# Optimization experiments

Measured on AMD Instinct MI355X. Metric: run time of the kernel, lower is better.

Reference implementation:

```python
import jax, jax.numpy as jnp
import numpy as np

EPS = 1e-5

def _layernorm(x, g, b):
    mu = jnp.mean(x, axis=-1, keepdims=True)
    var = jnp.mean((x - mu) ** 2, axis=-1, keepdims=True)
    return (x - mu) * jax.lax.rsqrt(var + EPS) * g + b

def setup_inputs() -> dict:
    key = jax.random.key(0)
    ks = jax.random.split(key, 12)
    B, N, C, n = 2, 1024, 256, 100
    x = jax.random.normal(ks[0], (B, N, C), dtype=jnp.float32)
    query = jax.random.normal(ks[1], (n, B, C), dtype=jnp.float32)
    policy = jax.random.uniform(ks[2], (B, N, 1), dtype=jnp.float32)
    s = lambda k, shp: jax.random.normal(k, shp, dtype=jnp.float32) * (1.0 / np.sqrt(shp[0]))
    return {
        "x": x, "query": query, "policy": policy,
        "ln_g": jnp.ones((C,), jnp.float32), "ln_b": jnp.zeros((C,), jnp.float32),
        "W_in": s(ks[3], (C, C)), "b_in": jnp.zeros((C,), jnp.float32),
        "W1": s(ks[4], (2 * C, C)), "b1": jnp.zeros((C,), jnp.float32),
        "W2": s(ks[5], (C, C // 2)), "b2": jnp.zeros((C // 2,), jnp.float32),
        "W3": s(ks[6], (C // 2, 2)), "b3": jnp.zeros((2,), jnp.float32),
    }

def reference(x, query, policy, ln_g, ln_b, W_in, b_in, W1, b1, W2, b2, W3, b3):
    B, N, C = x.shape
    n = query.shape[0]
    q = jnp.transpose(query, (1, 0, 2))  # [B, n, C]
    # in_conv: LayerNorm -> Linear -> GELU. The torch code repeats x across the
    # query dim first, but the math is identical per query, so compute once.
    h = jax.nn.gelu(_layernorm(x, ln_g, ln_b) @ W_in + b_in, approximate=False)  # [B, N, C]
    half = C // 2
    local_x = h[:, :, :half]  # [B, N, C/2]
    # policy-weighted masked pooling (policy identical across queries)
    glob = jnp.sum(h[:, :, half:] * policy, axis=1, keepdims=True) / jnp.sum(policy, axis=1, keepdims=True)  # [B, 1, C/2]
    feature = jnp.concatenate([
        jnp.broadcast_to(local_x[:, None, :, :], (B, n, N, half)),
        jnp.broadcast_to(glob[:, None, :, :], (B, n, N, half)),
        jnp.broadcast_to(q[:, :, None, :], (B, n, N, C)),
    ], axis=-1)  # [B, n, N, 2C]
    z = jax.nn.gelu(feature @ W1 + b1, approximate=False)
    z = jax.nn.gelu(z @ W2 + b2, approximate=False)
    z = z @ W3 + b3
    return jax.nn.log_softmax(z, axis=-1)  # [B, n, N, 2]
```

## Files before the change

### kernel.cpp

```cpp
#include <hip/hip_runtime.h>
#include <hip/hip_bf16.h>
#include <math.h>

#define BB 2
#define NN 1024
#define CC 256
#define NQ 100
#define HALF 128

typedef __attribute__((ext_vector_type(8))) short bf16x8;
typedef __attribute__((ext_vector_type(4))) float f32x4;

__device__ __forceinline__ float exp2_fast(float v) {
#if __has_builtin(__builtin_amdgcn_exp2f)
    return __builtin_amdgcn_exp2f(v);
#else
    return __expf(0.69314718056f * v);
#endif
}

__device__ __forceinline__ float gelu_fast(float x) {
    float x2 = x * x;
    float v = x * fmaf(0.10293942f, x2, 2.30211418f);
    float e = exp2_fast(v);
    float r = __builtin_amdgcn_rcpf(1.0f + e);
    return fmaf(-x, r, x);
}

__device__ __forceinline__ short f2bf(float f) {
    union { float f; unsigned u; } v; v.f = f;
    return (short)((v.u + 0x7FFFu + ((v.u >> 16) & 1u)) >> 16);
}

__global__ __launch_bounds__(256) void kA_fused(
        const float* __restrict__ x, const float* __restrict__ ln_g,
        const float* __restrict__ ln_b, const float* __restrict__ W_in,
        const float* __restrict__ b_in, const float* __restrict__ policy,
        const float* __restrict__ W1, float* __restrict__ At,
        float* __restrict__ gpart, float* __restrict__ ppart) {
    __shared__ float xst[CC][4];
    __shared__ float hst[HALF][4];
    int t = threadIdx.x;
    int wave = t >> 6, lane = t & 63;
    int blk = blockIdx.x;
    int row0 = blk * 4;
    const float* xr = x + (size_t)(row0 + wave) * CC;
    float v0 = xr[lane], v1 = xr[lane + 64], v2 = xr[lane + 128], v3 = xr[lane + 192];
    float s = v0 + v1 + v2 + v3;
    for (int off = 32; off; off >>= 1) s += __shfl_down(s, off);
    s = __shfl(s, 0);
    float mu = s * (1.0f / CC);
    float d0 = v0 - mu, d1 = v1 - mu, d2 = v2 - mu, d3 = v3 - mu;
    float vs = d0 * d0 + d1 * d1 + d2 * d2 + d3 * d3;
    for (int off = 32; off; off >>= 1) vs += __shfl_down(vs, off);
    vs = __shfl(vs, 0);
    float rstd = rsqrtf(vs * (1.0f / CC) + 1e-5f);
    xst[lane][wave]       = d0 * rstd * ln_g[lane]       + ln_b[lane];
    xst[lane + 64][wave]  = d1 * rstd * ln_g[lane + 64]  + ln_b[lane + 64];
    xst[lane + 128][wave] = d2 * rstd * ln_g[lane + 128] + ln_b[lane + 128];
    xst[lane + 192][wave] = d3 * rstd * ln_g[lane + 192] + ln_b[lane + 192];
    __syncthreads();
    float a0 = b_in[t], a1 = a0, a2 = a0, a3 = a0;
    #pragma unroll 8
    for (int k = 0; k < CC; ++k) {
        float4 xv = *(const float4*)xst[k];
        float wv = W_in[k * CC + t];
        a0 = fmaf(xv.x, wv, a0); a1 = fmaf(xv.y, wv, a1);
        a2 = fmaf(xv.z, wv, a2); a3 = fmaf(xv.w, wv, a3);
    }
    float h0 = gelu_fast(a0), h1 = gelu_fast(a1);
    float h2 = gelu_fast(a2), h3 = gelu_fast(a3);
    float p0 = policy[row0], p1 = policy[row0 + 1];
    float p2 = policy[row0 + 2], p3 = policy[row0 + 3];
    if (t < HALF) {
        hst[t][0] = h0; hst[t][1] = h1; hst[t][2] = h2; hst[t][3] = h3;
    } else {
        gpart[(size_t)blk * HALF + (t - HALF)] =
            h0 * p0 + h1 * p1 + h2 * p2 + h3 * p3;
    }
    if (t == 0) ppart[blk] = p0 + p1 + p2 + p3;
    __syncthreads();
    float c0 = 0, c1 = 0, c2 = 0, c3 = 0;
    #pragma unroll 8
    for (int k = 0; k < HALF; ++k) {
        float4 hv = *(const float4*)hst[k];
        float wv = W1[k * CC + t];
        c0 = fmaf(hv.x, wv, c0); c1 = fmaf(hv.y, wv, c1);
        c2 = fmaf(hv.z, wv, c2); c3 = fmaf(hv.w, wv, c3);
    }
    int b = row0 >> 10;
    int lr = row0 & (NN - 1);
    size_t tb = ((size_t)(b * 64 + (lr >> 4)) * 32 + (t >> 3)) * 128 + (t & 7);
    int r16 = lr & 15;
    At[tb + (r16 + 0) * 8] = c0;
    At[tb + (r16 + 1) * 8] = c1;
    At[tb + (r16 + 2) * 8] = c2;
    At[tb + (r16 + 3) * 8] = c3;
}

__global__ __launch_bounds__(256) void kB_qc_prep(
        const float* __restrict__ query, const float* __restrict__ W1,
        const float* __restrict__ W2, const float* __restrict__ gpart,
        const float* __restrict__ ppart, const float* __restrict__ b1,
        float* __restrict__ Qc, short* __restrict__ W2T) {
    int blk = blockIdx.x, t = threadIdx.x;
    if (blk >= BB * NQ) {
        int u = (blk - BB * NQ) * 256 + t;
        int n = u & 127;
        int kq = u >> 7;
        short4 v;
        v.x = f2bf(W2[(kq * 4 + 0) * HALF + n]);
        v.y = f2bf(W2[(kq * 4 + 1) * HALF + n]);
        v.z = f2bf(W2[(kq * 4 + 2) * HALF + n]);
        v.w = f2bf(W2[(kq * 4 + 3) * HALF + n]);
        *(short4*)(W2T + (size_t)((n >> 4) * 32 + (kq >> 1)) * 128
                   + (n & 15) * 8 + (kq & 1) * 4) = v;
        return;
    }
    __shared__ float gl2[2][HALF];
    __shared__ float gls[HALF];
    __shared__ float qs[CC];
    __shared__ float pss;
    int b = blk / NQ, i = blk % NQ;
    int c = t & 127, hh = t >> 7;
    {
        const float* gp = gpart + ((size_t)b * 256 + hh * 128) * HALF + c;
        float s = 0.f;
        #pragma unroll 16
        for (int ch = 0; ch < 128; ++ch) s += gp[(size_t)ch * HALF];
        gl2[hh][c] = s;
    }
    if (t < 64) {
        const float* pp = ppart + b * 256;
        float ps = pp[t] + pp[t + 64] + pp[t + 128] + pp[t + 192];
        for (int off = 32; off; off >>= 1) ps += __shfl_down(ps, off);
        if (t == 0) pss = ps;
    }
    qs[t] = query[(size_t)(i * BB + b) * CC + t];
    __syncthreads();
    if (t < HALF) gls[t] = (gl2[0][t] + gl2[1][t]) / pss;
    __syncthreads();
    float g = b1[t];
    #pragma unroll 8
    for (int k = 0; k < HALF; ++k)
        g = fmaf(gls[k], W1[(HALF + k) * CC + t], g);
    #pragma unroll 8
    for (int k = 0; k < CC; ++k)
        g = fmaf(qs[k], W1[(2 * HALF + k) * CC + t], g);
    Qc[(size_t)blk * CC + t] = g;
}

__global__ __launch_bounds__(256, 4) void k5_main(
        const float* __restrict__ At, const float* __restrict__ Qc,
        const short* __restrict__ W2T, const float* __restrict__ b2,
        const float* __restrict__ W3, const float* __restrict__ b3,
        float* __restrict__ out, int parity) {
    __shared__ short w2s[2][4096];

    int t = threadIdx.x;
    int lane = t & 63, w = t >> 6;
    int col16 = lane & 15, quad = lane >> 4;
    int blk = blockIdx.x * 2 + parity;
    int jt = blk & 7;
    int iq = (blk >> 3) % NQ;
    int b  = blk / (8 * NQ);
    const float* A0 = At + (size_t)(b * 64 + jt * 8 + w * 2) * 4096 + col16 * 8;
    const float* Qrow = Qc + (size_t)(b * NQ + iq) * CC;
    const short* Wg = W2T + (size_t)((t >> 6) * 32 + ((t >> 4) & 3)) * 128
                      + (t & 15) * 8;

    f32x4 acc[2][8];
    #pragma unroll
    for (int mi = 0; mi < 2; ++mi)
        #pragma unroll
        for (int ni = 0; ni < 8; ++ni)
            acc[mi][ni] = (f32x4){0.f, 0.f, 0.f, 0.f};

    bf16x8 nx0 = *(const bf16x8*)(Wg);
    bf16x8 nx1 = *(const bf16x8*)(Wg + 16384);
    float4 a00 = *(const float4*)(A0 + quad * 128);
    float4 a01 = *(const float4*)(A0 + quad * 128 + 4);
    float4 a10 = *(const float4*)(A0 + 4096 + quad * 128);
    float4 a11 = *(const float4*)(A0 + 4096 + quad * 128 + 4);
    float4 q0 = *(const float4*)(Qrow + quad * 8);
    float4 q1 = *(const float4*)(Qrow + quad * 8 + 4);
    *(bf16x8*)&w2s[0][t * 8] = nx0;
    *(bf16x8*)&w2s[0][2048 + t * 8] = nx1;
    nx0 = *(const bf16x8*)(Wg + 512);
    nx1 = *(const bf16x8*)(Wg + 16384 + 512);
    __syncthreads();

    #pragma unroll
    for (int kt = 0; kt < 8; ++kt) {
        int buf = kt & 1;
        if (kt < 7) {
            *(bf16x8*)&w2s[1 - buf][t * 8] = nx0;
            *(bf16x8*)&w2s[1 - buf][2048 + t * 8] = nx1;
        }
        if (kt < 6) {
            nx0 = *(const bf16x8*)(Wg + (kt + 2) * 512);
            nx1 = *(const bf16x8*)(Wg + 16384 + (kt + 2) * 512);
        }
        union { bf16x8 v; __hip_bfloat162 h[4]; } f0, f1;
        f0.h[0] = __float22bfloat162_rn(make_float2(gelu_fast(a00.x + q0.x),
                                                   gelu_fast(a00.y + q0.y)));
        f0.h[1] = __float22bfloat162_rn(make_float2(gelu_fast(a00.z + q0.z),
                                                   gelu_fast(a00.w + q0.w)));
        f0.h[2] = __float22bfloat162_rn(make_float2(gelu_fast(a01.x + q1.x),
                                                   gelu_fast(a01.y + q1.y)));
        f0.h[3] = __float22bfloat162_rn(make_float2(gelu_fast(a01.z + q1.z),
                                                   gelu_fast(a01.w + q1.w)));
        f1.h[0] = __float22bfloat162_rn(make_float2(gelu_fast(a10.x + q0.x),
                                                   gelu_fast(a10.y + q0.y)));
        f1.h[1] = __float22bfloat162_rn(make_float2(gelu_fast(a10.z + q0.z),
                                                   gelu_fast(a10.w + q0.w)));
        f1.h[2] = __float22bfloat162_rn(make_float2(gelu_fast(a11.x + q1.x),
                                                   gelu_fast(a11.y + q1.y)));
        f1.h[3] = __float22bfloat162_rn(make_float2(gelu_fast(a11.z + q1.z),
                                                   gelu_fast(a11.w + q1.w)));
        if (kt < 7) {
            const float* Ap = A0 + (size_t)((kt + 1) * 4 + quad) * 128;
            a00 = *(const float4*)(Ap);
            a01 = *(const float4*)(Ap + 4);
            a10 = *(const float4*)(Ap + 4096);
            a11 = *(const float4*)(Ap + 4096 + 4);
            q0 = *(const float4*)(Qrow + (kt + 1) * 32 + quad * 8);
            q1 = *(const float4*)(Qrow + (kt + 1) * 32 + quad * 8 + 4);
        }
        #pragma unroll
        for (int ni = 0; ni < 8; ++ni) {
            bf16x8 bv = *(const bf16x8*)&w2s[buf][(ni * 64 + lane) * 8];
            acc[0][ni] = __builtin_amdgcn_mfma_f32_16x16x32_bf16(f0.v, bv,
                                                                 acc[0][ni], 0, 0, 0);
            acc[1][ni] = __builtin_amdgcn_mfma_f32_16x16x32_bf16(f1.v, bv,
                                                                 acc[1][ni], 0, 0, 0);
        }
        if (kt < 7) __syncthreads();
    }

    float b30 = b3[0], b31 = b3[1];
    #pragma unroll
    for (int mi = 0; mi < 2; ++mi) {
        float p0[4] = {0, 0, 0, 0}, p1[4] = {0, 0, 0, 0};
        #pragma unroll
        for (int ni = 0; ni < 8; ++ni) {
            int c = ni * 16 + col16;
            float bb = b2[c];
            float2 w3v = *(const float2*)(W3 + c * 2);
            #pragma unroll
            for (int r = 0; r < 4; ++r) {
                float z = gelu_fast(acc[mi][ni][r] + bb);
                p0[r] = fmaf(z, w3v.x, p0[r]);
                p1[r] = fmaf(z, w3v.y, p1[r]);
            }
        }
        #pragma unroll
        for (int r = 0; r < 4; ++r) {
            float s0 = p0[r], s1 = p1[r];
            #pragma unroll
            for (int off = 1; off < 16; off <<= 1) {
                s0 += __shfl_xor(s0, off);
                s1 += __shfl_xor(s1, off);
            }
            if (col16 == 0) {
                float z0 = s0 + b30, z1v = s1 + b31;
                float m = fmaxf(z0, z1v);
                float lse = m + __logf(__expf(z0 - m) + __expf(z1v - m));
                int j = jt * 128 + w * 32 + mi * 16 + quad * 4 + r;
                *(float2*)(out + ((size_t)(b * NQ + iq) * NN + j) * 2) =
                    make_float2(z0 - lse, z1v - lse);
            }
        }
    }
}

extern "C" void kernel_launch(void* const* d_in, const int* in_sizes, int n_in,
                              void* d_out, int out_size, void* d_ws, size_t ws_size,
                              hipStream_t stream) {
    const float* x      = (const float*)d_in[0];
    const float* query  = (const float*)d_in[1];
    const float* policy = (const float*)d_in[2];
    const float* ln_g   = (const float*)d_in[3];
    const float* ln_b   = (const float*)d_in[4];
    const float* W_in   = (const float*)d_in[5];
    const float* b_in   = (const float*)d_in[6];
    const float* W1     = (const float*)d_in[7];
    const float* b1     = (const float*)d_in[8];
    const float* W2     = (const float*)d_in[9];
    const float* b2     = (const float*)d_in[10];
    const float* W3     = (const float*)d_in[11];
    const float* b3     = (const float*)d_in[12];
    float* out = (float*)d_out;

    float* ws    = (float*)d_ws;
    float* At    = ws;
    float* Qc    = ws + 524288;
    float* gpart = ws + 575488;
    float* ppart = ws + 641024;
    short* W2T   = (short*)(ws + 641536);

    kA_fused<<<512, 256, 0, stream>>>(x, ln_g, ln_b, W_in, b_in, policy,
                                      W1, At, gpart, ppart);
    kB_qc_prep<<<BB * NQ + 32, 256, 0, stream>>>(query, W1, W2, gpart, ppart,
                                                 b1, Qc, W2T);
    k5_main<<<800, 256, 0, stream>>>(At, Qc, W2T, b2, W3, b3, out, 0);
    k5_main<<<800, 256, 0, stream>>>(At, Qc, W2T, b2, W3, b3, out, 1);
}
```

Measured before the change: 167.4 us.

## Move query projection and W2 conversion into first kernel; merge main launches

```diff
diff --git a/kernel.cpp b/kernel.cpp
--- a/kernel.cpp
+++ b/kernel.cpp
@@ -36,13 +36,41 @@
         const float* __restrict__ x, const float* __restrict__ ln_g,
         const float* __restrict__ ln_b, const float* __restrict__ W_in,
         const float* __restrict__ b_in, const float* __restrict__ policy,
-        const float* __restrict__ W1, float* __restrict__ At,
-        float* __restrict__ gpart, float* __restrict__ ppart) {
+        const float* __restrict__ query, const float* __restrict__ W1,
+        const float* __restrict__ W2, float* __restrict__ At,
+        float* __restrict__ Qcq, float* __restrict__ gpart,
+        float* __restrict__ ppart, short* __restrict__ W2T) {
     __shared__ float xst[CC][4];
     __shared__ float hst[HALF][4];
     int t = threadIdx.x;
+    int blk = blockIdx.x;
+    if (blk >= 712) {
+        int u = (blk - 712) * 256 + t;
+        int n = u & 127;
+        int kq = u >> 7;
+        short4 v;
+        v.x = f2bf(W2[(kq * 4 + 0) * HALF + n]);
+        v.y = f2bf(W2[(kq * 4 + 1) * HALF + n]);
+        v.z = f2bf(W2[(kq * 4 + 2) * HALF + n]);
+        v.w = f2bf(W2[(kq * 4 + 3) * HALF + n]);
+        *(short4*)(W2T + (size_t)((n >> 4) * 32 + (kq >> 1)) * 128
+                   + (n & 15) * 8 + (kq & 1) * 4) = v;
+        return;
+    }
+    if (blk >= 512) {
+        float* qs = (float*)xst;
+        int row = blk - 512;
+        int b = row / NQ, i = row % NQ;
+        qs[t] = query[(size_t)(i * BB + b) * CC + t];
+        __syncthreads();
+        float g = 0.f;
+        #pragma unroll 8
+        for (int k = 0; k < CC; ++k)
+            g = fmaf(qs[k], W1[(2 * HALF + k) * CC + t], g);
+        Qcq[(size_t)row * CC + t] = g;
+        return;
+    }
     int wave = t >> 6, lane = t & 63;
-    int blk = blockIdx.x;
     int row0 = blk * 4;
     const float* xr = x + (size_t)(row0 + wave) * CC;
     float v0 = xr[lane], v1 = xr[lane + 64], v2 = xr[lane + 128], v3 = xr[lane + 192];
@@ -98,30 +126,14 @@
     At[tb + (r16 + 3) * 8] = c3;
 }
 
-__global__ __launch_bounds__(256) void kB_qc_prep(
-        const float* __restrict__ query, const float* __restrict__ W1,
-        const float* __restrict__ W2, const float* __restrict__ gpart,
+__global__ __launch_bounds__(256) void kB_gterm(
+        const float* __restrict__ W1, const float* __restrict__ gpart,
         const float* __restrict__ ppart, const float* __restrict__ b1,
-        float* __restrict__ Qc, short* __restrict__ W2T) {
-    int blk = blockIdx.x, t = threadIdx.x;
-    if (blk >= BB * NQ) {
-        int u = (blk - BB * NQ) * 256 + t;
-        int n = u & 127;
-        int kq = u >> 7;
-        short4 v;
-        v.x = f2bf(W2[(kq * 4 + 0) * HALF + n]);
-        v.y = f2bf(W2[(kq * 4 + 1) * HALF + n]);
-        v.z = f2bf(W2[(kq * 4 + 2) * HALF + n]);
-        v.w = f2bf(W2[(kq * 4 + 3) * HALF + n]);
-        *(short4*)(W2T + (size_t)((n >> 4) * 32 + (kq >> 1)) * 128
-                   + (n & 15) * 8 + (kq & 1) * 4) = v;
-        return;
-    }
+        float* __restrict__ Gterm) {
     __shared__ float gl2[2][HALF];
     __shared__ float gls[HALF];
-    __shared__ float qs[CC];
     __shared__ float pss;
-    int b = blk / NQ, i = blk % NQ;
+    int b = blockIdx.x, t = threadIdx.x;
     int c = t & 127, hh = t >> 7;
     {
         const float* gp = gpart + ((size_t)b * 256 + hh * 128) * HALF + c;
@@ -136,7 +148,6 @@
         for (int off = 32; off; off >>= 1) ps += __shfl_down(ps, off);
         if (t == 0) pss = ps;
     }
-    qs[t] = query[(size_t)(i * BB + b) * CC + t];
     __syncthreads();
     if (t < HALF) gls[t] = (gl2[0][t] + gl2[1][t]) / pss;
     __syncthreads();
@@ -144,28 +155,26 @@
     #pragma unroll 8
     for (int k = 0; k < HALF; ++k)
         g = fmaf(gls[k], W1[(HALF + k) * CC + t], g);
-    #pragma unroll 8
-    for (int k = 0; k < CC; ++k)
-        g = fmaf(qs[k], W1[(2 * HALF + k) * CC + t], g);
-    Qc[(size_t)blk * CC + t] = g;
+    Gterm[b * CC + t] = g;
 }
 
 __global__ __launch_bounds__(256, 4) void k5_main(
-        const float* __restrict__ At, const float* __restrict__ Qc,
-        const short* __restrict__ W2T, const float* __restrict__ b2,
-        const float* __restrict__ W3, const float* __restrict__ b3,
-        float* __restrict__ out, int parity) {
+        const float* __restrict__ At, const float* __restrict__ Qcq,
+        const float* __restrict__ Gterm, const short* __restrict__ W2T,
+        const float* __restrict__ b2, const float* __restrict__ W3,
+        const float* __restrict__ b3, float* __restrict__ out) {
     __shared__ short w2s[2][4096];
 
     int t = threadIdx.x;
     int lane = t & 63, w = t >> 6;
     int col16 = lane & 15, quad = lane >> 4;
-    int blk = blockIdx.x * 2 + parity;
+    int blk = blockIdx.x;
     int jt = blk & 7;
     int iq = (blk >> 3) % NQ;
     int b  = blk / (8 * NQ);
     const float* A0 = At + (size_t)(b * 64 + jt * 8 + w * 2) * 4096 + col16 * 8;
-    const float* Qrow = Qc + (size_t)(b * NQ + iq) * CC;
+    const float* Qrow = Qcq + (size_t)(b * NQ + iq) * CC;
+    const float* Grow = Gterm + b * CC;
     const short* Wg = W2T + (size_t)((t >> 6) * 32 + ((t >> 4) & 3)) * 128
                       + (t & 15) * 8;
 
@@ -184,6 +193,8 @@
     float4 a11 = *(const float4*)(A0 + 4096 + quad * 128 + 4);
     float4 q0 = *(const float4*)(Qrow + quad * 8);
     float4 q1 = *(const float4*)(Qrow + quad * 8 + 4);
+    float4 g0 = *(const float4*)(Grow + quad * 8);
+    float4 g1 = *(const float4*)(Grow + quad * 8 + 4);
     *(bf16x8*)&w2s[0][t * 8] = nx0;
     *(bf16x8*)&w2s[0][2048 + t * 8] = nx1;
     nx0 = *(const bf16x8*)(Wg + 512);
@@ -201,23 +212,27 @@
             nx0 = *(const bf16x8*)(Wg + (kt + 2) * 512);
             nx1 = *(const bf16x8*)(Wg + 16384 + (kt + 2) * 512);
         }
+        float qg0x = q0.x + g0.x, qg0y = q0.y + g0.y;
+        float qg0z = q0.z + g0.z, qg0w = q0.w + g0.w;
+        float qg1x = q1.x + g1.x, qg1y = q1.y + g1.y;
+        float qg1z = q1.z + g1.z, qg1w = q1.w + g1.w;
         union { bf16x8 v; __hip_bfloat162 h[4]; } f0, f1;
-        f0.h[0] = __float22bfloat162_rn(make_float2(gelu_fast(a00.x + q0.x),
-                                                   gelu_fast(a00.y + q0.y)));
-        f0.h[1] = __float22bfloat162_rn(make_float2(gelu_fast(a00.z + q0.z),
-                                                   gelu_fast(a00.w + q0.w)));
-        f0.h[2] = __float22bfloat162_rn(make_float2(gelu_fast(a01.x + q1.x),
-                                                   gelu_fast(a01.y + q1.y)));
-        f0.h[3] = __float22bfloat162_rn(make_float2(gelu_fast(a01.z + q1.z),
-                                                   gelu_fast(a01.w + q1.w)));
-        f1.h[0] = __float22bfloat162_rn(make_float2(gelu_fast(a10.x + q0.x),
-                                                   gelu_fast(a10.y + q0.y)));
-        f1.h[1] = __float22bfloat162_rn(make_float2(gelu_fast(a10.z + q0.z),
-                                                   gelu_fast(a10.w + q0.w)));
-        f1.h[2] = __float22bfloat162_rn(make_float2(gelu_fast(a11.x + q1.x),
-                                                   gelu_fast(a11.y + q1.y)));
-        f1.h[3] = __float22bfloat162_rn(make_float2(gelu_fast(a11.z + q1.z),
-                                                   gelu_fast(a11.w + q1.w)));
+        f0.h[0] = __float22bfloat162_rn(make_float2(gelu_fast(a00.x + qg0x),
+                                                   gelu_fast(a00.y + qg0y)));
+        f0.h[1] = __float22bfloat162_rn(make_float2(gelu_fast(a00.z + qg0z),
+                                                   gelu_fast(a00.w + qg0w)));
+        f0.h[2] = __float22bfloat162_rn(make_float2(gelu_fast(a01.x + qg1x),
+                                                   gelu_fast(a01.y + qg1y)));
+        f0.h[3] = __float22bfloat162_rn(make_float2(gelu_fast(a01.z + qg1z),
+                                                   gelu_fast(a01.w + qg1w)));
+        f1.h[0] = __float22bfloat162_rn(make_float2(gelu_fast(a10.x + qg0x),
+                                                   gelu_fast(a10.y + qg0y)));
+        f1.h[1] = __float22bfloat162_rn(make_float2(gelu_fast(a10.z + qg0z),
+                                                   gelu_fast(a10.w + qg0w)));
+        f1.h[2] = __float22bfloat162_rn(make_float2(gelu_fast(a11.x + qg1x),
+                                                   gelu_fast(a11.y + qg1y)));
+        f1.h[3] = __float22bfloat162_rn(make_float2(gelu_fast(a11.z + qg1z),
+                                                   gelu_fast(a11.w + qg1w)));
         if (kt < 7) {
             const float* Ap = A0 + (size_t)((kt + 1) * 4 + quad) * 128;
             a00 = *(const float4*)(Ap);
@@ -226,6 +241,8 @@
             a11 = *(const float4*)(Ap + 4096 + 4);
             q0 = *(const float4*)(Qrow + (kt + 1) * 32 + quad * 8);
             q1 = *(const float4*)(Qrow + (kt + 1) * 32 + quad * 8 + 4);
+            g0 = *(const float4*)(Grow + (kt + 1) * 32 + quad * 8);
+            g1 = *(const float4*)(Grow + (kt + 1) * 32 + quad * 8 + 4);
         }
         #pragma unroll
         for (int ni = 0; ni < 8; ++ni) {
@@ -294,15 +311,14 @@
 
     float* ws    = (float*)d_ws;
     float* At    = ws;
-    float* Qc    = ws + 524288;
+    float* Qcq   = ws + 524288;
     float* gpart = ws + 575488;
     float* ppart = ws + 641024;
     short* W2T   = (short*)(ws + 641536);
-
-    kA_fused<<<512, 256, 0, stream>>>(x, ln_g, ln_b, W_in, b_in, policy,
-                                      W1, At, gpart, ppart);
-    kB_qc_prep<<<BB * NQ + 32, 256, 0, stream>>>(query, W1, W2, gpart, ppart,
-                                                 b1, Qc, W2T);
-    k5_main<<<800, 256, 0, stream>>>(At, Qc, W2T, b2, W3, b3, out, 0);
-    k5_main<<<800, 256, 0, stream>>>(At, Qc, W2T, b2, W3, b3, out, 1);
-}
+    float* Gterm = ws + 657920;
+
+    kA_fused<<<744, 256, 0, stream>>>(x, ln_g, ln_b, W_in, b_in, policy,
+                                      query, W1, W2, At, Qcq, gpart, ppart, W2T);
+    kB_gterm<<<BB, 256, 0, stream>>>(W1, gpart, ppart, b1, Gterm);
+    k5_main<<<1600, 256, 0, stream>>>(At, Qcq, Gterm, W2T, b2, W3, b3, out);
+}
```

New measurement: 152.6 us (median of 2 runs). 1.1x faster.
